# Performance work log

Measured on AMD Instinct MI355X. Metric: run time of the kernel, lower is better.

The kernel has to match this reference:

```python
import jax, jax.numpy as jnp
import numpy as np

N, C, D, H = 4096, 64, 128, 4
CD = 2 * D          # combined_dim = 2*input_size
DQ = CD // 8        # per-head query/key dim


def _mlp(x, W1, b1, W2, b2):
    # MLP(in, hidden, out): Linear -> ReLU -> Linear
    return jax.nn.relu(x @ W1.T + b1) @ W2.T + b2


def _gru(x, h, Wih, bih, Whh, bhh):
    # torch.nn.GRUCell math
    gi = x @ Wih.T + bih
    gh = h @ Whh.T + bhh
    ir, iz, inn = jnp.split(gi, 3, axis=-1)
    hr, hz, hn = jnp.split(gh, 3, axis=-1)
    r = jax.nn.sigmoid(ir + hr)
    z = jax.nn.sigmoid(iz + hz)
    n = jnp.tanh(inn + r * hn)
    return (1.0 - z) * n + z * h


def setup_inputs() -> dict:
    key = jax.random.key(0)
    ks = jax.random.split(key, 16)
    def w(k, shape, fan):
        return jax.random.normal(k, shape, jnp.float32) / np.float32(np.sqrt(fan))
    return {
        "x": jax.random.normal(ks[0], (N, D), jnp.float32),
        "h": jax.random.normal(ks[1], (N, D), jnp.float32),
        "cluster_h": jax.random.normal(ks[2], (C, D), jnp.float32),
        "query_vectors": jax.random.normal(ks[3], (C, D), jnp.float32),
        "cluster_labels": jax.random.randint(ks[4], (N,), 0, C),
        "nodes_ind": jnp.arange(N),
        "edge_index_intra": jax.random.randint(ks[5], (2, 1024), 0, N),
        "num_clusters": C,
        "Wq": w(ks[6], (H, DQ, CD), CD), "bq": jnp.zeros((H, DQ), jnp.float32),
        "Wk": w(ks[7], (H, DQ, CD), CD), "bk": jnp.zeros((H, DQ), jnp.float32),
        "Wv": w(ks[8], (H, CD, CD), CD), "bv": jnp.zeros((H, CD), jnp.float32),
        "W1": w(ks[9], (CD, H * CD), H * CD), "b1": jnp.zeros((CD,), jnp.float32),
        "W2": w(ks[10], (CD, CD), CD), "b2": jnp.zeros((CD,), jnp.float32),
        "gru_Wih": w(ks[11], (3 * D, D), D), "gru_bih": jnp.zeros((3 * D,), jnp.float32),
        "gru_Whh": w(ks[12], (3 * D, D), D), "gru_bhh": jnp.zeros((3 * D,), jnp.float32),
        "Wp": 0.1 * w(ks[13], (D, D), D), "bp": jnp.zeros((D,), jnp.float32),
    }


def reference(x, h, cluster_h, query_vectors, cluster_labels, nodes_ind,
              edge_index_intra, num_clusters,
              Wq, bq, Wk, bk, Wv, bv, W1, b1, W2, b2,
              gru_Wih, gru_bih, gru_Whh, gru_bhh, Wp, bp):
    combined = jnp.concatenate([x, h], axis=-1)              # [N, 2D]
    # multi-head dense attention over all nodes (heads vectorized)
    q = jnp.einsum('nd,hed->hne', combined, Wq) + bq[:, None, :]   # [H,N,DQ]
    k = jnp.einsum('nd,hed->hne', combined, Wk) + bk[:, None, :]
    v = jnp.einsum('nd,hed->hne', combined, Wv) + bv[:, None, :]   # [H,N,2D]
    scores = jnp.einsum('hne,hme->hnm', q, k) / jnp.sqrt(jnp.float32(DQ))
    attn = jax.nn.softmax(jax.nn.leaky_relu(scores, 0.2), axis=-1)  # [H,N,N]
    hp = jnp.einsum('hnm,hme->hne', attn, v)                 # [H,N,2D]
    hp = jnp.transpose(hp, (1, 0, 2)).reshape(combined.shape[0], -1)  # [N,H*2D]
    node_repr = _mlp(hp, W1, b1, W2, b2) + combined          # [N,2D]
    # per-cluster mean of previous node hidden states
    ones = jnp.ones((h.shape[0],), h.dtype)
    counts = jax.ops.segment_sum(ones, cluster_labels, num_segments=num_clusters)
    sums = jax.ops.segment_sum(h, cluster_labels, num_segments=num_clusters)
    agg = sums / jnp.maximum(counts, 1.0)[:, None]           # [C,D]
    present = (counts > 0)[:, None]
    new_ch = _gru(agg, cluster_h, gru_Wih, gru_bih, gru_Whh, gru_bhh)
    updated_cluster_h = jnp.where(present, new_ch, cluster_h)  # [C,D]
    # cluster-to-node projection broadcast back to nodes
    c2n = (updated_cluster_h @ Wp.T + bp)[cluster_labels]    # [N,D]
    updated_h = node_repr[:, D:] + c2n                       # [N,D]
    return updated_h, updated_cluster_h
```

## Files before the change

kernel.cpp:

```cpp
#include <hip/hip_runtime.h>
#include <math.h>

#define N_NODES 4096
#define NHEADS  4
#define NSPLIT  4
#define KVRANGE 1024

typedef _Float16 f16;
typedef _Float16 half8 __attribute__((ext_vector_type(8)));
typedef float f32x4 __attribute__((ext_vector_type(4)));

__global__ __launch_bounds__(256) void k_combined(const float* __restrict__ x,
                                                  const float* __restrict__ h,
                                                  f16* __restrict__ comb16) {
  int i = blockIdx.x * blockDim.x + threadIdx.x;
  int n = i >> 6, c = i & 63;
  float4 v;
  if (c < 32) v = ((const float4*)x)[n * 32 + c];
  else        v = ((const float4*)h)[n * 32 + (c - 32)];
  union { uint2 u; f16 h4[4]; } pk;
  pk.h4[0] = (f16)v.x; pk.h4[1] = (f16)v.y; pk.h4[2] = (f16)v.z; pk.h4[3] = (f16)v.w;
  *(uint2*)&comb16[(size_t)i * 4] = pk.u;
}

__global__ __launch_bounds__(256) void k_w2h(const float* __restrict__ Wq,
                                             const float* __restrict__ Wk,
                                             const float* __restrict__ Wv,
                                             const float* __restrict__ W1,
                                             const float* __restrict__ W2,
                                             f16* __restrict__ pool) {
  int i4 = (blockIdx.x * 256 + threadIdx.x) * 4;
  const float* src; int off;
  if      (i4 <  32768) { src = Wq; off = 0; }
  else if (i4 <  65536) { src = Wk; off = 32768; }
  else if (i4 < 327680) { src = Wv; off = 65536; }
  else if (i4 < 589824) { src = W1; off = 327680; }
  else                  { src = W2; off = 589824; }
  float4 v = *(const float4*)&src[i4 - off];
  union { uint2 u; f16 h4[4]; } pk;
  pk.h4[0] = (f16)v.x; pk.h4[1] = (f16)v.y; pk.h4[2] = (f16)v.z; pk.h4[3] = (f16)v.w;
  *(uint2*)&pool[i4] = pk.u;
}

template <int EPI>
__global__ __launch_bounds__(256) void k_gemm16(const f16* __restrict__ A,
                                                const f16* __restrict__ B,
                                                const float* __restrict__ bias,
                                                const float* __restrict__ resid,
                                                const int* __restrict__ lab,
                                                const float* __restrict__ c2n,
                                                void* __restrict__ outv,
                                                int M, int K, int J, float alpha) {
  __shared__ f16 As[64 * 64];
  __shared__ f16 Bs[64 * 64];
  const int t  = threadIdx.x;
  const int mb = blockIdx.x * 64, jb = blockIdx.y * 64;
  const int w  = t >> 6, l = t & 63;
  const int g_ = l >> 4, c_ = l & 15;
  const int m0 = (w >> 1) * 32, n0 = (w & 1) * 32;

  f32x4 acc[2][2];
#pragma unroll
  for (int i = 0; i < 2; ++i)
#pragma unroll
    for (int j = 0; j < 2; ++j) acc[i][j] = (f32x4){0.f, 0.f, 0.f, 0.f};

#define FRAG16(BUF, row, kh) \
  (*(const half8*)&BUF[(size_t)(row) * 64 + (((((kh) * 4 + g_) ^ (c_ & 7))) << 3)])

  for (int kb = 0; kb < K; kb += 64) {
    __syncthreads();
#pragma unroll
    for (int i = 0; i < 2; ++i) {
      int f = t + i * 256;
      int r = f >> 3, ch = f & 7;
      *(uint4*)&As[r * 64 + ((ch ^ (r & 7)) << 3)] =
          *(const uint4*)&A[(size_t)(mb + r) * K + kb + ch * 8];
      *(uint4*)&Bs[r * 64 + ((ch ^ (r & 7)) << 3)] =
          *(const uint4*)&B[(size_t)(jb + r) * K + kb + ch * 8];
    }
    __syncthreads();
#pragma unroll
    for (int kh = 0; kh < 2; ++kh) {
      half8 a0 = FRAG16(As, m0 + c_, kh);
      half8 a1 = FRAG16(As, m0 + 16 + c_, kh);
      half8 b0 = FRAG16(Bs, n0 + c_, kh);
      half8 b1 = FRAG16(Bs, n0 + 16 + c_, kh);
      acc[0][0] = __builtin_amdgcn_mfma_f32_16x16x32_f16(a0, b0, acc[0][0], 0, 0, 0);
      acc[0][1] = __builtin_amdgcn_mfma_f32_16x16x32_f16(a0, b1, acc[0][1], 0, 0, 0);
      acc[1][0] = __builtin_amdgcn_mfma_f32_16x16x32_f16(a1, b0, acc[1][0], 0, 0, 0);
      acc[1][1] = __builtin_amdgcn_mfma_f32_16x16x32_f16(a1, b1, acc[1][1], 0, 0, 0);
    }
  }
#undef FRAG16

#pragma unroll
  for (int mt = 0; mt < 2; ++mt)
#pragma unroll
    for (int nt = 0; nt < 2; ++nt) {
      int mbase = mb + m0 + mt * 16 + g_ * 4;
      int jj    = jb + n0 + nt * 16 + c_;
      if (EPI == 0 || EPI == 1) {
        f16* out = (f16*)outv;
        float bc = bias[jj];
#pragma unroll
        for (int r = 0; r < 4; ++r) {
          float v = (acc[mt][nt][r] + bc) * alpha;
          if (EPI == 1) v = fmaxf(v, 0.f);
          out[(size_t)(mbase + r) * J + jj] = (f16)v;
        }
      } else if (EPI == 2) {
        f16* out = (f16*)outv;
#pragma unroll
        for (int r = 0; r < 4; ++r)
          out[(size_t)(mbase + r) * J + jj] = (f16)(acc[mt][nt][r] + bias[mbase + r]);
      } else {
        float* out = (float*)outv;
        float bc = bias[jj];
#pragma unroll
        for (int r = 0; r < 4; ++r) {
          int m = mbase + r;
          out[(size_t)m * J + jj] = acc[mt][nt][r] + bc +
              resid[(size_t)m * J + jj] + c2n[lab[m] * 128 + jj];
        }
      }
    }
}

__global__ __launch_bounds__(256, 3) void k_attn_mfma(const f16* __restrict__ qg,
                                                      const f16* __restrict__ kg,
                                                      const f16* __restrict__ vt,
                                                      f16* __restrict__ pO,
                                                      float* __restrict__ pM,
                                                      float* __restrict__ pL) {
  const int hd  = blockIdx.y;
  const int sp  = blockIdx.z;
  const int kv0 = sp * KVRANGE;
  const int t   = threadIdx.x;
  const int w   = t >> 6, l = t & 63;
  const int g   = l >> 4, c = l & 15;
  const int qb  = blockIdx.x * 64;

  __shared__ f16 Ks[32 * 40];
  __shared__ f16 Vs[256 * 40];
  __shared__ f16 Ps[64 * 40];
  __shared__ float CfS[64];

  half8 qf = *(const half8*)&qg[(size_t)(qb + w * 16 + c) * 128 + hd * 32 + g * 8];

  f32x4 oacc[4][4];
#pragma unroll
  for (int i = 0; i < 4; ++i)
#pragma unroll
    for (int j = 0; j < 4; ++j) oacc[i][j] = (f32x4){0.f, 0.f, 0.f, 0.f};
  float m_run = -INFINITY, l_run = 0.f;
  const f32x4 zero4 = {0.f, 0.f, 0.f, 0.f};

  for (int kb = 0; kb < KVRANGE; kb += 32) {
    __syncthreads();
    if (t < 128) {
      int r = t >> 2, c8 = (t & 3) * 8;
      *(uint4*)&Ks[r * 40 + c8] =
          *(const uint4*)&kg[(size_t)(kv0 + kb + r) * 128 + hd * 32 + c8];
    }
#pragma unroll
    for (int i = 0; i < 4; ++i) {
      int cc = i * 256 + t, d = cc >> 2, c8 = (cc & 3) * 8;
      *(uint4*)&Vs[d * 40 + c8] =
          *(const uint4*)&vt[(size_t)(hd * 256 + d) * 4096 + kv0 + kb + c8];
    }
    __syncthreads();

    f32x4 s0 = __builtin_amdgcn_mfma_f32_16x16x32_f16(
        *(const half8*)&Ks[(c) * 40 + g * 8], qf, zero4, 0, 0, 0);
    f32x4 s1 = __builtin_amdgcn_mfma_f32_16x16x32_f16(
        *(const half8*)&Ks[(16 + c) * 40 + g * 8], qf, zero4, 0, 0, 0);

    float sv[8];
#pragma unroll
    for (int r = 0; r < 4; ++r) {
      float a = s0[r]; sv[r]     = a > 0.f ? a : 0.2f * a;
      float b = s1[r]; sv[4 + r] = b > 0.f ? b : 0.2f * b;
    }
    float mx = sv[0];
#pragma unroll
    for (int r = 1; r < 8; ++r) mx = fmaxf(mx, sv[r]);
    mx = fmaxf(mx, __shfl_xor(mx, 16));
    mx = fmaxf(mx, __shfl_xor(mx, 32));

    float cf = 1.f;
    if (!__all(mx <= m_run + 8.f)) {
      float m_new = fmaxf(m_run, mx);
      cf = __expf(m_run - m_new);
      m_run = m_new;
    }
    float p[8], ps = 0.f;
#pragma unroll
    for (int r = 0; r < 8; ++r) { p[r] = __expf(sv[r] - m_run); ps += p[r]; }
    ps += __shfl_xor(ps, 16);
    ps += __shfl_xor(ps, 32);
    l_run = l_run * cf + ps;

    if (g == 0) CfS[w * 16 + c] = cf;
    {
      union { unsigned u; f16 h2[2]; } z;
      uint2 lo, hi;
      z.h2[0] = (f16)p[0]; z.h2[1] = (f16)p[1]; lo.x = z.u;
      z.h2[0] = (f16)p[2]; z.h2[1] = (f16)p[3]; lo.y = z.u;
      z.h2[0] = (f16)p[4]; z.h2[1] = (f16)p[5]; hi.x = z.u;
      z.h2[0] = (f16)p[6]; z.h2[1] = (f16)p[7]; hi.y = z.u;
      *(uint2*)&Ps[(w * 16 + c) * 40 + g * 4]      = lo;
      *(uint2*)&Ps[(w * 16 + c) * 40 + 16 + g * 4] = hi;
    }
    __syncthreads();

#pragma unroll
    for (int qt = 0; qt < 4; ++qt) {
      float cfq = CfS[qt * 16 + c];
      if (!__all(cfq == 1.f)) {
#pragma unroll
        for (int i = 0; i < 4; ++i) {
          oacc[i][qt][0] *= cfq; oacc[i][qt][1] *= cfq;
          oacc[i][qt][2] *= cfq; oacc[i][qt][3] *= cfq;
        }
      }
    }
    half8 pfr[4];
#pragma unroll
    for (int qt = 0; qt < 4; ++qt)
      pfr[qt] = *(const half8*)&Ps[(qt * 16 + c) * 40 + g * 8];
#pragma unroll
    for (int i = 0; i < 4; ++i) {
      half8 vfr = *(const half8*)&Vs[((w * 4 + i) * 16 + c) * 40 + g * 8];
#pragma unroll
      for (int qt = 0; qt < 4; ++qt)
        oacc[i][qt] = __builtin_amdgcn_mfma_f32_16x16x32_f16(vfr, pfr[qt], oacc[i][qt], 0, 0, 0);
    }
  }

  __syncthreads();
  if (g == 0) CfS[w * 16 + c] = l_run;
  __syncthreads();
  float linv[4];
#pragma unroll
  for (int qt = 0; qt < 4; ++qt) linv[qt] = 1.f / CfS[qt * 16 + c];
#pragma unroll
  for (int i = 0; i < 4; ++i)
#pragma unroll
    for (int qt = 0; qt < 4; ++qt)
#pragma unroll
      for (int r = 0; r < 4; ++r) {
        int j = hd * 256 + (w * 4 + i) * 16 + g * 4 + r;
        pO[(size_t)(sp * 1024 + j) * 4096 + qb + qt * 16 + c] =
            (f16)(oacc[i][qt][r] * linv[qt]);
      }
  if (g == 0) {
    pM[(sp * 4 + hd) * 4096 + qb + w * 16 + c] = m_run;
    pL[(sp * 4 + hd) * 4096 + qb + w * 16 + c] = l_run;
  }
}

__global__ __launch_bounds__(256) void k_merge(const f16* __restrict__ pO,
                                               const float* __restrict__ pM,
                                               const float* __restrict__ pL,
                                               f16* __restrict__ hp) {
  const int q0 = blockIdx.x * 64, jb = blockIdx.y * 64;
  const int h  = jb >> 8;
  const int t  = threadIdx.x;
  __shared__ float wm[NSPLIT][64], wl[NSPLIT][64];
  __shared__ float tile[64][65];

  if (t < 64) {
#pragma unroll
    for (int s = 0; s < NSPLIT; ++s) {
      wm[s][t] = pM[(s * 4 + h) * 4096 + q0 + t];
      wl[s][t] = pL[(s * 4 + h) * 4096 + q0 + t];
    }
  }
  __syncthreads();

  const int q8 = (t & 7) * 8;
#pragma unroll
  for (int it = 0; it < 2; ++it) {
    int jl = (t >> 3) + it * 32;
    float wgt[NSPLIT][8], inv[8];
#pragma unroll
    for (int q = 0; q < 8; ++q) {
      float M = wm[0][q8 + q];
#pragma unroll
      for (int s = 1; s < NSPLIT; ++s) M = fmaxf(M, wm[s][q8 + q]);
      float den = 0.f;
#pragma unroll
      for (int s = 0; s < NSPLIT; ++s) {
        float wv = wl[s][q8 + q] * __expf(wm[s][q8 + q] - M);
        wgt[s][q] = wv; den += wv;
      }
      inv[q] = 1.f / den;
    }
    float o[8] = {0.f};
#pragma unroll
    for (int s = 0; s < NSPLIT; ++s) {
      union { uint4 u; f16 h8[8]; } raw;
      raw.u = *(const uint4*)&pO[(size_t)(s * 1024 + jb + jl) * 4096 + q0 + q8];
#pragma unroll
      for (int q = 0; q < 8; ++q) o[q] += wgt[s][q] * (float)raw.h8[q];
    }
#pragma unroll
    for (int q = 0; q < 8; ++q) tile[q8 + q][jl] = o[q] * inv[q];
  }
  __syncthreads();

#pragma unroll
  for (int it = 0; it < 2; ++it) {
    int ql = (t >> 3) + it * 32, chk = t & 7;
    union { uint4 u; f16 h8[8]; } pk;
#pragma unroll
    for (int k = 0; k < 8; ++k) pk.h8[k] = (f16)tile[ql][chk * 8 + k];
    *(uint4*)&hp[(size_t)(q0 + ql) * 1024 + jb + chk * 8] = pk.u;
  }
}

__global__ void k_zero(float* __restrict__ p, int n) {
  int i = blockIdx.x * blockDim.x + threadIdx.x;
  if (i < n) p[i] = 0.f;
}

__global__ __launch_bounds__(256) void k_segsum(const float* __restrict__ h,
                                                const int* __restrict__ lab,
                                                float* __restrict__ sums,
                                                float* __restrict__ cnt) {
  int i = blockIdx.x * blockDim.x + threadIdx.x;
  int n = i >> 7, d = i & 127;
  int c = lab[n];
  atomicAdd(&sums[c * 128 + d], h[i]);
  if (d == 0) atomicAdd(&cnt[c], 1.0f);
}

__global__ __launch_bounds__(128) void k_gru(const float* __restrict__ sums,
                                             const float* __restrict__ cnt,
                                             const float* __restrict__ ch,
                                             const float* __restrict__ Wih,
                                             const float* __restrict__ bih,
                                             const float* __restrict__ Whh,
                                             const float* __restrict__ bhh,
                                             float* __restrict__ uch,
                                             float* __restrict__ out_uch) {
  int c = blockIdx.x, d = threadIdx.x;
  __shared__ float ax[128], hx[128];
  float count = cnt[c];
  ax[d] = sums[c * 128 + d] / fmaxf(count, 1.0f);
  hx[d] = ch[c * 128 + d];
  __syncthreads();
  float gi[3], gh[3];
#pragma unroll
  for (int g = 0; g < 3; ++g) {
    const float4* wi4 = (const float4*)&Wih[(size_t)(g * 128 + d) * 128];
    const float4* wh4 = (const float4*)&Whh[(size_t)(g * 128 + d) * 128];
    float si = 0.f, sh = 0.f;
#pragma unroll 8
    for (int e = 0; e < 32; ++e) {
      float4 wv = wi4[e], hv = wh4[e];
      si = fmaf(ax[e*4+0], wv.x, si); si = fmaf(ax[e*4+1], wv.y, si);
      si = fmaf(ax[e*4+2], wv.z, si); si = fmaf(ax[e*4+3], wv.w, si);
      sh = fmaf(hx[e*4+0], hv.x, sh); sh = fmaf(hx[e*4+1], hv.y, sh);
      sh = fmaf(hx[e*4+2], hv.z, sh); sh = fmaf(hx[e*4+3], hv.w, sh);
    }
    gi[g] = si + bih[g * 128 + d];
    gh[g] = sh + bhh[g * 128 + d];
  }
  float r = 1.f / (1.f + expf(-(gi[0] + gh[0])));
  float z = 1.f / (1.f + expf(-(gi[1] + gh[1])));
  float nn = tanhf(gi[2] + r * gh[2]);
  float hv = hx[d];
  float nh = (1.f - z) * nn + z * hv;
  float res = (count > 0.f) ? nh : hv;
  uch[c * 128 + d] = res;
  out_uch[c * 128 + d] = res;
}

__global__ __launch_bounds__(128) void k_c2n(const float* __restrict__ uch,
                                             const float* __restrict__ Wp,
                                             const float* __restrict__ bp,
                                             float* __restrict__ c2n) {
  int c = blockIdx.x, d = threadIdx.x;
  __shared__ float u[128];
  u[d] = uch[c * 128 + d];
  __syncthreads();
  const float4* w4 = (const float4*)&Wp[(size_t)d * 128];
  float s = 0.f;
#pragma unroll 8
  for (int e = 0; e < 32; ++e) {
    float4 wv = w4[e];
    s = fmaf(u[e*4+0], wv.x, s); s = fmaf(u[e*4+1], wv.y, s);
    s = fmaf(u[e*4+2], wv.z, s); s = fmaf(u[e*4+3], wv.w, s);
  }
  c2n[c * 128 + d] = s + bp[d];
}

extern "C" void kernel_launch(void* const* d_in, const int* in_sizes, int n_in,
                              void* d_out, int out_size, void* d_ws, size_t ws_size,
                              hipStream_t stream) {
  const float* x    = (const float*)d_in[0];
  const float* h    = (const float*)d_in[1];
  const float* ch   = (const float*)d_in[2];
  const int*   lab  = (const int*)d_in[4];
  const float* Wq   = (const float*)d_in[8];
  const float* bq   = (const float*)d_in[9];
  const float* Wk   = (const float*)d_in[10];
  const float* bk   = (const float*)d_in[11];
  const float* Wv   = (const float*)d_in[12];
  const float* bv   = (const float*)d_in[13];
  const float* W1   = (const float*)d_in[14];
  const float* b1   = (const float*)d_in[15];
  const float* W2   = (const float*)d_in[16];
  const float* b2   = (const float*)d_in[17];
  const float* gWih = (const float*)d_in[18];
  const float* gbih = (const float*)d_in[19];
  const float* gWhh = (const float*)d_in[20];
  const float* gbhh = (const float*)d_in[21];
  const float* Wp   = (const float*)d_in[22];
  const float* bp   = (const float*)d_in[23];

  float* outp    = (float*)d_out;
  float* out_uch = outp + 4096 * 128;

  f16* comb16 = (f16*)d_ws;
  f16* w16    = comb16 + 4096 * 256;
  f16* wq16   = w16;
  f16* wk16   = w16 + 32768;
  f16* wv16   = w16 + 65536;
  f16* w116   = w16 + 327680;
  f16* w216   = w16 + 589824;
  f16* qf16   = w16 + 655360;
  f16* kf16   = qf16 + 4096 * 128;
  f16* vt16   = kf16 + 4096 * 128;
  f16* pO     = vt16 + 1024 * 4096;
  f16* hp16   = pO + (size_t)NSPLIT * 1024 * 4096;
  f16* y116   = hp16 + (size_t)4096 * 1024;
  float* pM   = (float*)(y116 + 4096 * 256);
  float* pL   = pM + NSPLIT * 4 * 4096;
  float* sums = pL + NSPLIT * 4 * 4096;
  float* cnt  = sums + 64 * 128;
  float* uch  = cnt + 64;
  float* c2n  = uch + 64 * 128;

  const float qscale = 0.17677669529663687f;

  k_combined<<<1024, 256, 0, stream>>>(x, h, comb16);
  k_w2h<<<640, 256, 0, stream>>>(Wq, Wk, Wv, W1, W2, w16);
  k_gemm16<0><<<dim3(64, 2),  256, 0, stream>>>(comb16, wq16, bq, nullptr, nullptr, nullptr, qf16, 4096, 256, 128,  qscale);
  k_gemm16<0><<<dim3(64, 2),  256, 0, stream>>>(comb16, wk16, bk, nullptr, nullptr, nullptr, kf16, 4096, 256, 128,  1.0f);
  k_gemm16<2><<<dim3(16, 64), 256, 0, stream>>>(wv16, comb16, bv, nullptr, nullptr, nullptr, vt16, 1024, 256, 4096, 1.0f);
  k_attn_mfma<<<dim3(64, NHEADS, NSPLIT), 256, 0, stream>>>(qf16, kf16, vt16, pO, pM, pL);
  k_merge<<<dim3(64, 16), 256, 0, stream>>>(pO, pM, pL, hp16);
  k_gemm16<1><<<dim3(64, 4), 256, 0, stream>>>(hp16, w116, b1, nullptr, nullptr, nullptr, y116, 4096, 1024, 256, 1.0f);
  k_zero<<<33, 256, 0, stream>>>(sums, 64 * 128 + 64);
  k_segsum<<<2048, 256, 0, stream>>>(h, lab, sums, cnt);
  k_gru<<<64, 128, 0, stream>>>(sums, cnt, ch, gWih, gbih, gWhh, gbhh, uch, out_uch);
  k_c2n<<<64, 128, 0, stream>>>(uch, Wp, bp, c2n);
  k_gemm16<3><<<dim3(64, 2), 256, 0, stream>>>(y116, w216 + 128 * 256, b2 + 128, h, lab, c2n, outp, 4096, 256, 128, 1.0f);
}
```

Measured before the change: 270.8 us.

## Merge small independent kernels into fewer heterogeneous launches

Cuts the launch sequence from 13 kernels to 6. The independent stages now share launches, with the block index picking the work: f16 conversion plus zeroing in one kernel, Q/K/V GEMMs plus segment-sum atomics in one, and attention merge plus GRU plus cluster projection in one. This removes per-launch overhead and the idle gaps between the many tiny serial kernels. In exchange, mixed-role kernels share register and shared-memory budgets, and their workloads may be unbalanced.

```diff
diff --git a/kernel.cpp b/kernel.cpp
--- a/kernel.cpp
+++ b/kernel.cpp
@@ -10,36 +10,90 @@
 typedef _Float16 half8 __attribute__((ext_vector_type(8)));
 typedef float f32x4 __attribute__((ext_vector_type(4)));
 
-__global__ __launch_bounds__(256) void k_combined(const float* __restrict__ x,
-                                                  const float* __restrict__ h,
-                                                  f16* __restrict__ comb16) {
-  int i = blockIdx.x * blockDim.x + threadIdx.x;
-  int n = i >> 6, c = i & 63;
-  float4 v;
-  if (c < 32) v = ((const float4*)x)[n * 32 + c];
-  else        v = ((const float4*)h)[n * 32 + (c - 32)];
-  union { uint2 u; f16 h4[4]; } pk;
-  pk.h4[0] = (f16)v.x; pk.h4[1] = (f16)v.y; pk.h4[2] = (f16)v.z; pk.h4[3] = (f16)v.w;
-  *(uint2*)&comb16[(size_t)i * 4] = pk.u;
-}
-
-__global__ __launch_bounds__(256) void k_w2h(const float* __restrict__ Wq,
-                                             const float* __restrict__ Wk,
-                                             const float* __restrict__ Wv,
-                                             const float* __restrict__ W1,
-                                             const float* __restrict__ W2,
-                                             f16* __restrict__ pool) {
-  int i4 = (blockIdx.x * 256 + threadIdx.x) * 4;
-  const float* src; int off;
-  if      (i4 <  32768) { src = Wq; off = 0; }
-  else if (i4 <  65536) { src = Wk; off = 32768; }
-  else if (i4 < 327680) { src = Wv; off = 65536; }
-  else if (i4 < 589824) { src = W1; off = 327680; }
-  else                  { src = W2; off = 589824; }
-  float4 v = *(const float4*)&src[i4 - off];
-  union { uint2 u; f16 h4[4]; } pk;
-  pk.h4[0] = (f16)v.x; pk.h4[1] = (f16)v.y; pk.h4[2] = (f16)v.z; pk.h4[3] = (f16)v.w;
-  *(uint2*)&pool[i4] = pk.u;
+template <int EPI>
+__device__ __forceinline__ void gemm_body(const f16* __restrict__ A,
+                                          const f16* __restrict__ B,
+                                          const float* __restrict__ bias,
+                                          const float* __restrict__ resid,
+                                          const int* __restrict__ lab,
+                                          const float* __restrict__ c2n,
+                                          void* __restrict__ outv,
+                                          int M, int K, int J, float alpha,
+                                          int bx, int by, f16* smem) {
+  f16* As = smem;
+  f16* Bs = smem + 64 * 64;
+  const int t  = threadIdx.x;
+  const int mb = bx * 64, jb = by * 64;
+  const int w  = t >> 6, l = t & 63;
+  const int g_ = l >> 4, c_ = l & 15;
+  const int m0 = (w >> 1) * 32, n0 = (w & 1) * 32;
+
+  f32x4 acc[2][2];
+#pragma unroll
+  for (int i = 0; i < 2; ++i)
+#pragma unroll
+    for (int j = 0; j < 2; ++j) acc[i][j] = (f32x4){0.f, 0.f, 0.f, 0.f};
+
+#define FRAG16(BUF, row, kh) \
+  (*(const half8*)&BUF[(size_t)(row) * 64 + (((((kh) * 4 + g_) ^ (c_ & 7))) << 3)])
+
+  for (int kb = 0; kb < K; kb += 64) {
+    __syncthreads();
+#pragma unroll
+    for (int i = 0; i < 2; ++i) {
+      int f = t + i * 256;
+      int r = f >> 3, ch = f & 7;
+      *(uint4*)&As[r * 64 + ((ch ^ (r & 7)) << 3)] =
+          *(const uint4*)&A[(size_t)(mb + r) * K + kb + ch * 8];
+      *(uint4*)&Bs[r * 64 + ((ch ^ (r & 7)) << 3)] =
+          *(const uint4*)&B[(size_t)(jb + r) * K + kb + ch * 8];
+    }
+    __syncthreads();
+#pragma unroll
+    for (int kh = 0; kh < 2; ++kh) {
+      half8 a0 = FRAG16(As, m0 + c_, kh);
+      half8 a1 = FRAG16(As, m0 + 16 + c_, kh);
+      half8 b0 = FRAG16(Bs, n0 + c_, kh);
+      half8 b1 = FRAG16(Bs, n0 + 16 + c_, kh);
+      acc[0][0] = __builtin_amdgcn_mfma_f32_16x16x32_f16(a0, b0, acc[0][0], 0, 0, 0);
+      acc[0][1] = __builtin_amdgcn_mfma_f32_16x16x32_f16(a0, b1, acc[0][1], 0, 0, 0);
+      acc[1][0] = __builtin_amdgcn_mfma_f32_16x16x32_f16(a1, b0, acc[1][0], 0, 0, 0);
+      acc[1][1] = __builtin_amdgcn_mfma_f32_16x16x32_f16(a1, b1, acc[1][1], 0, 0, 0);
+    }
+  }
+#undef FRAG16
+
+#pragma unroll
+  for (int mt = 0; mt < 2; ++mt)
+#pragma unroll
+    for (int nt = 0; nt < 2; ++nt) {
+      int mbase = mb + m0 + mt * 16 + g_ * 4;
+      int jj    = jb + n0 + nt * 16 + c_;
+      if (EPI == 0 || EPI == 1) {
+        f16* out = (f16*)outv;
+        float bc = bias[jj];
+#pragma unroll
+        for (int r = 0; r < 4; ++r) {
+          float v = (acc[mt][nt][r] + bc) * alpha;
+          if (EPI == 1) v = fmaxf(v, 0.f);
+          out[(size_t)(mbase + r) * J + jj] = (f16)v;
+        }
+      } else if (EPI == 2) {
+        f16* out = (f16*)outv;
+#pragma unroll
+        for (int r = 0; r < 4; ++r)
+          out[(size_t)(mbase + r) * J + jj] = (f16)(acc[mt][nt][r] + bias[mbase + r]);
+      } else {
+        float* out = (float*)outv;
+        float bc = bias[jj];
+#pragma unroll
+        for (int r = 0; r < 4; ++r) {
+          int m = mbase + r;
+          out[(size_t)m * J + jj] = acc[mt][nt][r] + bc +
+              resid[(size_t)m * J + jj] + c2n[lab[m] * 128 + jj];
+        }
+      }
+    }
 }
 
 template <int EPI>
@@ -51,80 +105,84 @@
                                                 const float* __restrict__ c2n,
                                                 void* __restrict__ outv,
                                                 int M, int K, int J, float alpha) {
-  __shared__ f16 As[64 * 64];
-  __shared__ f16 Bs[64 * 64];
-  const int t  = threadIdx.x;
-  const int mb = blockIdx.x * 64, jb = blockIdx.y * 64;
-  const int w  = t >> 6, l = t & 63;
-  const int g_ = l >> 4, c_ = l & 15;
-  const int m0 = (w >> 1) * 32, n0 = (w & 1) * 32;
-
-  f32x4 acc[2][2];
-#pragma unroll
-  for (int i = 0; i < 2; ++i)
-#pragma unroll
-    for (int j = 0; j < 2; ++j) acc[i][j] = (f32x4){0.f, 0.f, 0.f, 0.f};
-
-#define FRAG16(BUF, row, kh) \
-  (*(const half8*)&BUF[(size_t)(row) * 64 + (((((kh) * 4 + g_) ^ (c_ & 7))) << 3)])
-
-  for (int kb = 0; kb < K; kb += 64) {
-    __syncthreads();
-#pragma unroll
-    for (int i = 0; i < 2; ++i) {
-      int f = t + i * 256;
-      int r = f >> 3, ch = f & 7;
-      *(uint4*)&As[r * 64 + ((ch ^ (r & 7)) << 3)] =
-          *(const uint4*)&A[(size_t)(mb + r) * K + kb + ch * 8];
-      *(uint4*)&Bs[r * 64 + ((ch ^ (r & 7)) << 3)] =
-          *(const uint4*)&B[(size_t)(jb + r) * K + kb + ch * 8];
-    }
-    __syncthreads();
-#pragma unroll
-    for (int kh = 0; kh < 2; ++kh) {
-      half8 a0 = FRAG16(As, m0 + c_, kh);
-      half8 a1 = FRAG16(As, m0 + 16 + c_, kh);
-      half8 b0 = FRAG16(Bs, n0 + c_, kh);
-      half8 b1 = FRAG16(Bs, n0 + 16 + c_, kh);
-      acc[0][0] = __builtin_amdgcn_mfma_f32_16x16x32_f16(a0, b0, acc[0][0], 0, 0, 0);
-      acc[0][1] = __builtin_amdgcn_mfma_f32_16x16x32_f16(a0, b1, acc[0][1], 0, 0, 0);
-      acc[1][0] = __builtin_amdgcn_mfma_f32_16x16x32_f16(a1, b0, acc[1][0], 0, 0, 0);
-      acc[1][1] = __builtin_amdgcn_mfma_f32_16x16x32_f16(a1, b1, acc[1][1], 0, 0, 0);
-    }
-  }
-#undef FRAG16
-
-#pragma unroll
-  for (int mt = 0; mt < 2; ++mt)
-#pragma unroll
-    for (int nt = 0; nt < 2; ++nt) {
-      int mbase = mb + m0 + mt * 16 + g_ * 4;
-      int jj    = jb + n0 + nt * 16 + c_;
-      if (EPI == 0 || EPI == 1) {
-        f16* out = (f16*)outv;
-        float bc = bias[jj];
-#pragma unroll
-        for (int r = 0; r < 4; ++r) {
-          float v = (acc[mt][nt][r] + bc) * alpha;
-          if (EPI == 1) v = fmaxf(v, 0.f);
-          out[(size_t)(mbase + r) * J + jj] = (f16)v;
-        }
-      } else if (EPI == 2) {
-        f16* out = (f16*)outv;
-#pragma unroll
-        for (int r = 0; r < 4; ++r)
-          out[(size_t)(mbase + r) * J + jj] = (f16)(acc[mt][nt][r] + bias[mbase + r]);
-      } else {
-        float* out = (float*)outv;
-        float bc = bias[jj];
-#pragma unroll
-        for (int r = 0; r < 4; ++r) {
-          int m = mbase + r;
-          out[(size_t)m * J + jj] = acc[mt][nt][r] + bc +
-              resid[(size_t)m * J + jj] + c2n[lab[m] * 128 + jj];
-        }
-      }
-    }
+  __shared__ f16 smem[2 * 64 * 64];
+  gemm_body<EPI>(A, B, bias, resid, lab, c2n, outv, M, K, J, alpha,
+                 blockIdx.x, blockIdx.y, smem);
+}
+
+__global__ __launch_bounds__(256) void k_prep(const float* __restrict__ x,
+                                              const float* __restrict__ h,
+                                              const float* __restrict__ Wq,
+                                              const float* __restrict__ Wk,
+                                              const float* __restrict__ Wv,
+                                              const float* __restrict__ W1,
+                                              const float* __restrict__ W2,
+                                              f16* __restrict__ comb16,
+                                              f16* __restrict__ pool,
+                                              float* __restrict__ sums) {
+  const int b = blockIdx.x, t = threadIdx.x;
+  if (b < 1024) {
+    int i = b * 256 + t;
+    int n = i >> 6, c = i & 63;
+    float4 v;
+    if (c < 32) v = ((const float4*)x)[n * 32 + c];
+    else        v = ((const float4*)h)[n * 32 + (c - 32)];
+    union { uint2 u; f16 h4[4]; } pk;
+    pk.h4[0] = (f16)v.x; pk.h4[1] = (f16)v.y; pk.h4[2] = (f16)v.z; pk.h4[3] = (f16)v.w;
+    *(uint2*)&comb16[(size_t)i * 4] = pk.u;
+  } else if (b < 1664) {
+    int i4 = ((b - 1024) * 256 + t) * 4;
+    const float* src; int off;
+    if      (i4 <  32768) { src = Wq; off = 0; }
+    else if (i4 <  65536) { src = Wk; off = 32768; }
+    else if (i4 < 327680) { src = Wv; off = 65536; }
+    else if (i4 < 589824) { src = W1; off = 327680; }
+    else                  { src = W2; off = 589824; }
+    float4 v = *(const float4*)&src[i4 - off];
+    union { uint2 u; f16 h4[4]; } pk;
+    pk.h4[0] = (f16)v.x; pk.h4[1] = (f16)v.y; pk.h4[2] = (f16)v.z; pk.h4[3] = (f16)v.w;
+    *(uint2*)&pool[i4] = pk.u;
+  } else {
+    int i = (b - 1664) * 256 + t;
+    if (i < 8256) sums[i] = 0.f;
+  }
+}
+
+__global__ __launch_bounds__(256) void k_qkv(const f16* __restrict__ comb16,
+                                             const f16* __restrict__ wq16,
+                                             const f16* __restrict__ wk16,
+                                             const f16* __restrict__ wv16,
+                                             const float* __restrict__ bq,
+                                             const float* __restrict__ bk,
+                                             const float* __restrict__ bv,
+                                             f16* __restrict__ qf16,
+                                             f16* __restrict__ kf16,
+                                             f16* __restrict__ vt16,
+                                             const float* __restrict__ h,
+                                             const int* __restrict__ lab,
+                                             float* __restrict__ sums,
+                                             float* __restrict__ cnt,
+                                             float qscale) {
+  __shared__ f16 smem[2 * 64 * 64];
+  const int b = blockIdx.x;
+  if (b < 1024) {
+    gemm_body<2>(wv16, comb16, bv, nullptr, nullptr, nullptr, vt16,
+                 1024, 256, 4096, 1.0f, b & 15, b >> 4, smem);
+  } else if (b < 1152) {
+    int r = b - 1024;
+    gemm_body<0>(comb16, wq16, bq, nullptr, nullptr, nullptr, qf16,
+                 4096, 256, 128, qscale, r & 63, r >> 6, smem);
+  } else if (b < 1280) {
+    int r = b - 1152;
+    gemm_body<0>(comb16, wk16, bk, nullptr, nullptr, nullptr, kf16,
+                 4096, 256, 128, 1.0f, r & 63, r >> 6, smem);
+  } else {
+    int i = (b - 1280) * 256 + threadIdx.x;
+    int n = i >> 7, d = i & 127;
+    int c = lab[n];
+    atomicAdd(&sums[c * 128 + d], h[i]);
+    if (d == 0) atomicAdd(&cnt[c], 1.0f);
+  }
 }
 
 __global__ __launch_bounds__(256, 3) void k_attn_mfma(const f16* __restrict__ qg,
@@ -260,141 +318,120 @@
   }
 }
 
-__global__ __launch_bounds__(256) void k_merge(const f16* __restrict__ pO,
-                                               const float* __restrict__ pM,
-                                               const float* __restrict__ pL,
-                                               f16* __restrict__ hp) {
-  const int q0 = blockIdx.x * 64, jb = blockIdx.y * 64;
-  const int h  = jb >> 8;
-  const int t  = threadIdx.x;
-  __shared__ float wm[NSPLIT][64], wl[NSPLIT][64];
-  __shared__ float tile[64][65];
-
-  if (t < 64) {
-#pragma unroll
-    for (int s = 0; s < NSPLIT; ++s) {
-      wm[s][t] = pM[(s * 4 + h) * 4096 + q0 + t];
-      wl[s][t] = pL[(s * 4 + h) * 4096 + q0 + t];
-    }
-  }
-  __syncthreads();
-
-  const int q8 = (t & 7) * 8;
-#pragma unroll
-  for (int it = 0; it < 2; ++it) {
-    int jl = (t >> 3) + it * 32;
-    float wgt[NSPLIT][8], inv[8];
-#pragma unroll
-    for (int q = 0; q < 8; ++q) {
-      float M = wm[0][q8 + q];
-#pragma unroll
-      for (int s = 1; s < NSPLIT; ++s) M = fmaxf(M, wm[s][q8 + q]);
-      float den = 0.f;
+__global__ __launch_bounds__(256) void k_mergeplus(const f16* __restrict__ pO,
+                                                   const float* __restrict__ pM,
+                                                   const float* __restrict__ pL,
+                                                   f16* __restrict__ hp,
+                                                   const float* __restrict__ sums,
+                                                   const float* __restrict__ cnt,
+                                                   const float* __restrict__ ch,
+                                                   const float* __restrict__ gWih,
+                                                   const float* __restrict__ gbih,
+                                                   const float* __restrict__ gWhh,
+                                                   const float* __restrict__ gbhh,
+                                                   const float* __restrict__ Wp,
+                                                   const float* __restrict__ bp,
+                                                   float* __restrict__ out_uch,
+                                                   float* __restrict__ c2n) {
+  const int b = blockIdx.x, t = threadIdx.x;
+  if (b < 1024) {
+    __shared__ float wm[NSPLIT][64], wl[NSPLIT][64];
+    __shared__ float tile[64][65];
+    const int q0 = (b & 63) * 64, jb = (b >> 6) * 64;
+    const int h  = jb >> 8;
+
+    if (t < 64) {
 #pragma unroll
       for (int s = 0; s < NSPLIT; ++s) {
-        float wv = wl[s][q8 + q] * __expf(wm[s][q8 + q] - M);
-        wgt[s][q] = wv; den += wv;
-      }
-      inv[q] = 1.f / den;
-    }
-    float o[8] = {0.f};
-#pragma unroll
-    for (int s = 0; s < NSPLIT; ++s) {
-      union { uint4 u; f16 h8[8]; } raw;
-      raw.u = *(const uint4*)&pO[(size_t)(s * 1024 + jb + jl) * 4096 + q0 + q8];
-#pragma unroll
-      for (int q = 0; q < 8; ++q) o[q] += wgt[s][q] * (float)raw.h8[q];
-    }
-#pragma unroll
-    for (int q = 0; q < 8; ++q) tile[q8 + q][jl] = o[q] * inv[q];
-  }
-  __syncthreads();
-
-#pragma unroll
-  for (int it = 0; it < 2; ++it) {
-    int ql = (t >> 3) + it * 32, chk = t & 7;
-    union { uint4 u; f16 h8[8]; } pk;
-#pragma unroll
-    for (int k = 0; k < 8; ++k) pk.h8[k] = (f16)tile[ql][chk * 8 + k];
-    *(uint4*)&hp[(size_t)(q0 + ql) * 1024 + jb + chk * 8] = pk.u;
-  }
-}
-
-__global__ void k_zero(float* __restrict__ p, int n) {
-  int i = blockIdx.x * blockDim.x + threadIdx.x;
-  if (i < n) p[i] = 0.f;
-}
-
-__global__ __launch_bounds__(256) void k_segsum(const float* __restrict__ h,
-                                                const int* __restrict__ lab,
-                                                float* __restrict__ sums,
-                                                float* __restrict__ cnt) {
-  int i = blockIdx.x * blockDim.x + threadIdx.x;
-  int n = i >> 7, d = i & 127;
-  int c = lab[n];
-  atomicAdd(&sums[c * 128 + d], h[i]);
-  if (d == 0) atomicAdd(&cnt[c], 1.0f);
-}
-
-__global__ __launch_bounds__(128) void k_gru(const float* __restrict__ sums,
-                                             const float* __restrict__ cnt,
-                                             const float* __restrict__ ch,
-                                             const float* __restrict__ Wih,
-                                             const float* __restrict__ bih,
-                                             const float* __restrict__ Whh,
-                                             const float* __restrict__ bhh,
-                                             float* __restrict__ uch,
-                                             float* __restrict__ out_uch) {
-  int c = blockIdx.x, d = threadIdx.x;
-  __shared__ float ax[128], hx[128];
-  float count = cnt[c];
-  ax[d] = sums[c * 128 + d] / fmaxf(count, 1.0f);
-  hx[d] = ch[c * 128 + d];
-  __syncthreads();
-  float gi[3], gh[3];
-#pragma unroll
-  for (int g = 0; g < 3; ++g) {
-    const float4* wi4 = (const float4*)&Wih[(size_t)(g * 128 + d) * 128];
-    const float4* wh4 = (const float4*)&Whh[(size_t)(g * 128 + d) * 128];
-    float si = 0.f, sh = 0.f;
+        wm[s][t] = pM[(s * 4 + h) * 4096 + q0 + t];
+        wl[s][t] = pL[(s * 4 + h) * 4096 + q0 + t];
+      }
+    }
+    __syncthreads();
+
+    const int q8 = (t & 7) * 8;
+#pragma unroll
+    for (int it = 0; it < 2; ++it) {
+      int jl = (t >> 3) + it * 32;
+      float wgt[NSPLIT][8], inv[8];
+#pragma unroll
+      for (int q = 0; q < 8; ++q) {
+        float M = wm[0][q8 + q];
+#pragma unroll
+        for (int s = 1; s < NSPLIT; ++s) M = fmaxf(M, wm[s][q8 + q]);
+        float den = 0.f;
+#pragma unroll
+        for (int s = 0; s < NSPLIT; ++s) {
+          float wv = wl[s][q8 + q] * __expf(wm[s][q8 + q] - M);
+          wgt[s][q] = wv; den += wv;
+        }
+        inv[q] = 1.f / den;
+      }
+      float o[8] = {0.f};
+#pragma unroll
+      for (int s = 0; s < NSPLIT; ++s) {
+        union { uint4 u; f16 h8[8]; } raw;
+        raw.u = *(const uint4*)&pO[(size_t)(s * 1024 + jb + jl) * 4096 + q0 + q8];
+#pragma unroll
+        for (int q = 0; q < 8; ++q) o[q] += wgt[s][q] * (float)raw.h8[q];
+      }
+#pragma unroll
+      for (int q = 0; q < 8; ++q) tile[q8 + q][jl] = o[q] * inv[q];
+    }
+    __syncthreads();
+
+#pragma unroll
+    for (int it = 0; it < 2; ++it) {
+      int ql = (t >> 3) + it * 32, chk = t & 7;
+      union { uint4 u; f16 h8[8]; } pk;
+#pragma unroll
+      for (int k = 0; k < 8; ++k) pk.h8[k] = (f16)tile[ql][chk * 8 + k];
+      *(uint4*)&hp[(size_t)(q0 + ql) * 1024 + jb + chk * 8] = pk.u;
+    }
+  } else {
+    __shared__ float ax[2][128], hx[2][128], ul[2][128];
+    const int cc = t >> 7, d = t & 127;
+    const int c  = (b - 1024) * 2 + cc;
+    float count = cnt[c];
+    ax[cc][d] = sums[c * 128 + d] / fmaxf(count, 1.0f);
+    hx[cc][d] = ch[c * 128 + d];
+    __syncthreads();
+    float gi[3], gh[3];
+#pragma unroll
+    for (int g = 0; g < 3; ++g) {
+      const float4* wi4 = (const float4*)&gWih[(size_t)(g * 128 + d) * 128];
+      const float4* wh4 = (const float4*)&gWhh[(size_t)(g * 128 + d) * 128];
+      float si = 0.f, sh = 0.f;
+#pragma unroll 8
+      for (int e = 0; e < 32; ++e) {
+        float4 wv = wi4[e], hv = wh4[e];
+        si = fmaf(ax[cc][e*4+0], wv.x, si); si = fmaf(ax[cc][e*4+1], wv.y, si);
+        si = fmaf(ax[cc][e*4+2], wv.z, si); si = fmaf(ax[cc][e*4+3], wv.w, si);
+        sh = fmaf(hx[cc][e*4+0], hv.x, sh); sh = fmaf(hx[cc][e*4+1], hv.y, sh);
+        sh = fmaf(hx[cc][e*4+2], hv.z, sh); sh = fmaf(hx[cc][e*4+3], hv.w, sh);
+      }
+      gi[g] = si + gbih[g * 128 + d];
+      gh[g] = sh + gbhh[g * 128 + d];
+    }
+    float r = 1.f / (1.f + expf(-(gi[0] + gh[0])));
+    float z = 1.f / (1.f + expf(-(gi[1] + gh[1])));
+    float nn = tanhf(gi[2] + r * gh[2]);
+    float hv = hx[cc][d];
+    float nh = (1.f - z) * nn + z * hv;
+    float res = (count > 0.f) ? nh : hv;
+    ul[cc][d] = res;
+    out_uch[c * 128 + d] = res;
+    __syncthreads();
+    const float4* w4 = (const float4*)&Wp[(size_t)d * 128];
+    float s = 0.f;
 #pragma unroll 8
     for (int e = 0; e < 32; ++e) {
-      float4 wv = wi4[e], hv = wh4[e];
-      si = fmaf(ax[e*4+0], wv.x, si); si = fmaf(ax[e*4+1], wv.y, si);
-      si = fmaf(ax[e*4+2], wv.z, si); si = fmaf(ax[e*4+3], wv.w, si);
-      sh = fmaf(hx[e*4+0], hv.x, sh); sh = fmaf(hx[e*4+1], hv.y, sh);
-      sh = fmaf(hx[e*4+2], hv.z, sh); sh = fmaf(hx[e*4+3], hv.w, sh);
-    }
-    gi[g] = si + bih[g * 128 + d];
-    gh[g] = sh + bhh[g * 128 + d];
-  }
-  float r = 1.f / (1.f + expf(-(gi[0] + gh[0])));
-  float z = 1.f / (1.f + expf(-(gi[1] + gh[1])));
-  float nn = tanhf(gi[2] + r * gh[2]);
-  float hv = hx[d];
-  float nh = (1.f - z) * nn + z * hv;
-  float res = (count > 0.f) ? nh : hv;
-  uch[c * 128 + d] = res;
-  out_uch[c * 128 + d] = res;
-}
-
-__global__ __launch_bounds__(128) void k_c2n(const float* __restrict__ uch,
-                                             const float* __restrict__ Wp,
-                                             const float* __restrict__ bp,
-                                             float* __restrict__ c2n) {
-  int c = blockIdx.x, d = threadIdx.x;
-  __shared__ float u[128];
-  u[d] = uch[c * 128 + d];
-  __syncthreads();
-  const float4* w4 = (const float4*)&Wp[(size_t)d * 128];
-  float s = 0.f;
-#pragma unroll 8
-  for (int e = 0; e < 32; ++e) {
-    float4 wv = w4[e];
-    s = fmaf(u[e*4+0], wv.x, s); s = fmaf(u[e*4+1], wv.y, s);
-    s = fmaf(u[e*4+2], wv.z, s); s = fmaf(u[e*4+3], wv.w, s);
-  }
-  c2n[c * 128 + d] = s + bp[d];
+      float4 wv = w4[e];
+      s = fmaf(ul[cc][e*4+0], wv.x, s); s = fmaf(ul[cc][e*4+1], wv.y, s);
+      s = fmaf(ul[cc][e*4+2], wv.z, s); s = fmaf(ul[cc][e*4+3], wv.w, s);
+    }
+    c2n[c * 128 + d] = s + bp[d];
+  }
 }
 
 extern "C" void kernel_launch(void* const* d_in, const int* in_sizes, int n_in,
@@ -441,22 +478,18 @@
   float* pL   = pM + NSPLIT * 4 * 4096;
   float* sums = pL + NSPLIT * 4 * 4096;
   float* cnt  = sums + 64 * 128;
-  float* uch  = cnt + 64;
-  float* c2n  = uch + 64 * 128;
+  float* c2n  = cnt + 64;
 
   const float qscale = 0.17677669529663687f;
 
-  k_combined<<<1024, 256, 0, stream>>>(x, h, comb16);
-  k_w2h<<<640, 256, 0, stream>>>(Wq, Wk, Wv, W1, W2, w16);
-  k_gemm16<0><<<dim3(64, 2),  256, 0, stream>>>(comb16, wq16, bq, nullptr, nullptr, nullptr, qf16, 4096, 256, 128,  qscale);
-  k_gemm16<0><<<dim3(64, 2),  256, 0, stream>>>(comb16, wk16, bk, nullptr, nullptr, nullptr, kf16, 4096, 256, 128,  1.0f);
-  k_gemm16<2><<<dim3(16, 64), 256, 0, stream>>>(wv16, comb16, bv, nullptr, nullptr, nullptr, vt16, 1024, 256, 4096, 1.0f);
+  k_prep<<<1697, 256, 0, stream>>>(x, h, Wq, Wk, Wv, W1, W2, comb16, w16, sums);
+  k_qkv<<<3328, 256, 0, stream>>>(comb16, wq16, wk16, wv16, bq, bk, bv,
+                                  qf16, kf16, vt16, h, lab, sums, cnt, qscale);
   k_attn_mfma<<<dim3(64, NHEADS, NSPLIT), 256, 0, stream>>>(qf16, kf16, vt16, pO, pM, pL);
-  k_merge<<<dim3(64, 16), 256, 0, stream>>>(pO, pM, pL, hp16);
-  k_gemm16<1><<<dim3(64, 4), 256, 0, stream>>>(hp16, w116, b1, nullptr, nullptr, nullptr, y116, 4096, 1024, 256, 1.0f);
-  k_zero<<<33, 256, 0, stream>>>(sums, 64 * 128 + 64);
-  k_segsum<<<2048, 256, 0, stream>>>(h, lab, sums, cnt);
-  k_gru<<<64, 128, 0, stream>>>(sums, cnt, ch, gWih, gbih, gWhh, gbhh, uch, out_uch);
-  k_c2n<<<64, 128, 0, stream>>>(uch, Wp, bp, c2n);
-  k_gemm16<3><<<dim3(64, 2), 256, 0, stream>>>(y116, w216 + 128 * 256, b2 + 128, h, lab, c2n, outp, 4096, 256, 128, 1.0f);
-}
+  k_mergeplus<<<1056, 256, 0, stream>>>(pO, pM, pL, hp16, sums, cnt, ch,
+                                        gWih, gbih, gWhh, gbhh, Wp, bp, out_uch, c2n);
+  k_gemm16<1><<<dim3(64, 4), 256, 0, stream>>>(hp16, w116, b1, nullptr, nullptr, nullptr,
+                                               y116, 4096, 1024, 256, 1.0f);
+  k_gemm16<3><<<dim3(64, 2), 256, 0, stream>>>(y116, w216 + 128 * 256, b2 + 128, h, lab, c2n,
+                                               outp, 4096, 256, 128, 1.0f);
+}
```

New measurement: 259.5 us. 4.2% less time.
